# Kernel tuning notes

Hardware: AMD Instinct MI355X
Metric: run time of the kernel (lower is better)

The kernel has to match this reference:

```python
import jax, jax.numpy as jnp
import numpy as np

BLOCK_SIZE = 2

def setup_inputs() -> dict:
    key = jax.random.key(0)
    k0, k1 = jax.random.split(key)
    x0 = jax.random.normal(k0, (16, 64, 256, 256), dtype=jnp.float32)
    x1 = jax.random.normal(k1, (16,), dtype=jnp.float32)
    return {"x0": x0, "x1": x1}

def reference(x0, x1):
    # Faithful space-to-depth: NCHW -> N, C*bs^2, H/bs, W/bs
    # Element order in the depth dim is (h_inner, w_inner, c), matching the
    # original permute/split/reshape/stack chain.
    bs = BLOCK_SIZE
    B, C, H, W = x0.shape
    Ho, Wo = H // bs, W // bs
    y = jnp.transpose(x0, (0, 2, 3, 1))                 # [B,H,W,C]
    y = y.reshape(B, Ho, bs, Wo, bs, C)                  # split H and W into blocks
    y = jnp.transpose(y, (0, 1, 3, 2, 4, 5))             # [B,Ho,Wo,h_in,w_in,C]
    y = y.reshape(B, Ho, Wo, bs * bs * C)                # depth = (h_in, w_in, c)
    y = jnp.transpose(y, (0, 3, 1, 2))                   # [B, C*bs^2, Ho, Wo]
    return (y, x1)
```

## Files before the change

kernel.cpp:

```cpp
#include <hip/hip_runtime.h>


typedef float v4f __attribute__((ext_vector_type(4)));

constexpr long long Y_ELEMS  = 67108864;
constexpr long long S1_OFF4  = 262144;

__global__ void __launch_bounds__(256) s2d_kernel(const v4f* __restrict__ in,
                                                  const float* __restrict__ x1,
                                                  v4f* __restrict__ out) {
    long long t = (long long)blockIdx.x * blockDim.x + threadIdx.x;

    int wo4 = (int)(t & 31);
    int ho  = (int)((t >> 5) & 127);
    int c   = (int)((t >> 12) & 63);
    int hin = (int)((t >> 18) & 1);
    int b   = (int)(t >> 19);

    long long irow = (((long long)b * 64 + c) * 256 + (2 * ho + hin));
    long long i4   = irow * 64 + (wo4 << 1);
    v4f v0 = in[i4];
    v4f v1 = in[i4 + 1];

    long long o4 = (((long long)(b * 256 + hin * 128 + c)) * 128 + ho) * 32 + wo4;

    v4f s0 = {v0.x, v0.z, v1.x, v1.z};
    v4f s1 = {v0.y, v0.w, v1.y, v1.w};

    out[o4]           = s0;
    out[o4 + S1_OFF4] = s1;

    if (blockIdx.x == 0 && threadIdx.x < 16) {
        ((float*)out)[Y_ELEMS + threadIdx.x] = x1[threadIdx.x];
    }
}

extern "C" void kernel_launch(void* const* d_in, const int* in_sizes, int n_in,
                              void* d_out, int out_size, void* d_ws, size_t ws_size,
                              hipStream_t stream) {
    const v4f*   x0 = (const v4f*)d_in[0];
    const float* x1 = (const float*)d_in[1];
    v4f* out = (v4f*)d_out;

    const int block = 256;
    const int grid  = 32768;
    s2d_kernel<<<grid, block, 0, stream>>>(x0, x1, out);
}
```

Baseline: 97.13 us.

## Stage space-to-depth tiles through shared memory for contiguous output writes

Each block now loads a 16-row tile of one input channel plane, de-interleaves the even and odd columns into two shared-memory buffers, and then writes whole output row segments from them. Each wave writes a longer contiguous stretch of one output plane, and the grid is halved so each thread does twice the work. The cost is an extra shared-memory round trip and a barrier in a kernel that was already close to memory-bandwidth bound.

```diff
diff --git a/kernel.cpp b/kernel.cpp
--- a/kernel.cpp
+++ b/kernel.cpp
@@ -3,35 +3,60 @@
 
 typedef float v4f __attribute__((ext_vector_type(4)));
 
-constexpr long long Y_ELEMS  = 67108864;
-constexpr long long S1_OFF4  = 262144;
+constexpr long long Y_ELEMS = 67108864;
 
 __global__ void __launch_bounds__(256) s2d_kernel(const v4f* __restrict__ in,
                                                   const float* __restrict__ x1,
                                                   v4f* __restrict__ out) {
-    long long t = (long long)blockIdx.x * blockDim.x + threadIdx.x;
+    __shared__ float A[16 * 128];
+    __shared__ float B[16 * 128];
 
-    int wo4 = (int)(t & 31);
-    int ho  = (int)((t >> 5) & 127);
-    int c   = (int)((t >> 12) & 63);
-    int hin = (int)((t >> 18) & 1);
-    int b   = (int)(t >> 19);
+    int T = blockIdx.x;
+    int hblk = T & 15;
+    int c    = (T >> 4) & 63;
+    int b    = T >> 10;
 
-    long long irow = (((long long)b * 64 + c) * 256 + (2 * ho + hin));
-    long long i4   = irow * 64 + (wo4 << 1);
-    v4f v0 = in[i4];
-    v4f v1 = in[i4 + 1];
+    long long tile_base4 = (((long long)(b * 64 + c)) * 256 + hblk * 16) * 64;
 
-    long long o4 = (((long long)(b * 256 + hin * 128 + c)) * 128 + ho) * 32 + wo4;
+    int tid = threadIdx.x;
 
-    v4f s0 = {v0.x, v0.z, v1.x, v1.z};
-    v4f s1 = {v0.y, v0.w, v1.y, v1.w};
+    #pragma unroll
+    for (int it = 0; it < 2; ++it) {
+        int p  = tid + it * 256;
+        int hl = p >> 5;
+        int wp = p & 31;
+        long long i4 = tile_base4 + (long long)hl * 64 + (wp << 1);
+        v4f v0 = in[i4];
+        v4f v1 = in[i4 + 1];
+        v4f s0 = {v0.x, v0.z, v1.x, v1.z};
+        v4f s1 = {v0.y, v0.w, v1.y, v1.w};
+        *reinterpret_cast<v4f*>(&A[hl * 128 + (wp << 2)]) = s0;
+        *reinterpret_cast<v4f*>(&B[hl * 128 + (wp << 2)]) = s1;
+    }
 
-    out[o4]           = s0;
-    out[o4 + S1_OFF4] = s1;
+    __syncthreads();
 
-    if (blockIdx.x == 0 && threadIdx.x < 16) {
-        ((float*)out)[Y_ELEMS + threadIdx.x] = x1[threadIdx.x];
+    int s   = tid >> 6;
+    int l   = tid & 63;
+    int win = s >> 1;
+    int hin = s & 1;
+    int d   = hin * 128 + win * 64 + c;
+    int ho0 = hblk * 8;
+
+    const float* buf = win ? B : A;
+    long long obase4 = (((long long)(b * 256 + d)) * 128 + ho0) * 32;
+
+    #pragma unroll
+    for (int it = 0; it < 4; ++it) {
+        int f    = l + it * 64;
+        int ho_l = f >> 5;
+        int wo4  = f & 31;
+        v4f v = *reinterpret_cast<const v4f*>(&buf[(ho_l * 2 + hin) * 128 + (wo4 << 2)]);
+        out[obase4 + f] = v;
+    }
+
+    if (blockIdx.x == 0 && tid < 16) {
+        ((float*)out)[Y_ELEMS + tid] = x1[tid];
     }
 }
 
@@ -43,6 +68,6 @@
     v4f* out = (v4f*)d_out;
 
     const int block = 256;
-    const int grid  = 32768;
+    const int grid  = 16384;
     s2d_kernel<<<grid, block, 0, stream>>>(x0, x1, out);
 }
```

Result: slower. 99.99 us (+3.0%).
